# Kernel tuning notes

Measured on AMD Instinct MI355X. Metric: run time of the kernel, lower is better.

## Reference

```python
import jax, jax.numpy as jnp
import numpy as np

N_HEAD = 16
WINDOW = 128
CAUSAL = False


def setup_inputs() -> dict:
    key = jax.random.key(0)
    ks = jax.random.split(key, 5)
    B, T, D = 1, 4096, 1024
    x = jax.random.normal(ks[0], (B, T, D), dtype=jnp.float32)
    w_in = jax.random.normal(ks[1], (3 * D, D), dtype=jnp.float32) * 0.02
    b_in = jax.random.normal(ks[2], (3 * D,), dtype=jnp.float32) * 0.02
    w_out = jax.random.normal(ks[3], (D, D), dtype=jnp.float32) * 0.02
    b_out = jax.random.normal(ks[4], (D,), dtype=jnp.float32) * 0.02
    return {"x": x, "w_in": w_in, "b_in": b_in, "w_out": w_out, "b_out": b_out}


def _window_attention(x, w_in, b_in, w_out, b_out):
    B, T, D = x.shape
    H = N_HEAD
    hd = D // H
    scale = 1.0 / jnp.sqrt(jnp.float32(hd))

    # fused in-projection, as in torch nn.MultiheadAttention (y = x @ W^T + b)
    qkv = jnp.einsum('btd,ed->bte', x, w_in) + b_in  # (B, T, 3D)
    q, k, v = jnp.split(qkv, 3, axis=-1)
    # (B, H, T, hd)
    q = q.reshape(B, T, H, hd).transpose(0, 2, 1, 3)
    k = k.reshape(B, T, H, hd).transpose(0, 2, 1, 3)
    v = v.reshape(B, T, H, hd).transpose(0, 2, 1, 3)

    scores = jnp.einsum('bhqd,bhkd->bhqk', q, k) * scale  # (B, H, T, T)

    idx = jnp.arange(T)
    diff = idx[:, None] - idx[None, :]
    if CAUSAL:
        allowed = (diff >= 0) & (diff <= WINDOW)
    else:
        allowed = jnp.abs(diff) <= WINDOW
    NEG = jnp.float32(-1e30)
    scores = jnp.where(allowed[None, None, :, :], scores, NEG)

    attn = jax.nn.softmax(scores, axis=-1)
    ctx = jnp.einsum('bhqk,bhkd->bhqd', attn, v)  # (B, H, T, hd)
    ctx = ctx.transpose(0, 2, 1, 3).reshape(B, T, D)
    out = jnp.einsum('btd,ed->bte', ctx, w_out) + b_out
    return x + out  # residual, as in the module


def reference(x, w_in, b_in, w_out, b_out):
    return _window_attention(x, w_in, b_in, w_out, b_out)
```

## Files before the change

kernel.cpp:

```cpp
#include <hip/hip_runtime.h>

#define T_SEQ 4096
#define DMODEL 1024
#define NHEAD 16
#define HDIM 64
#define WIN 128

typedef __attribute__((ext_vector_type(8))) short bf16x8;
typedef __attribute__((ext_vector_type(4))) float f32x4;
typedef __attribute__((ext_vector_type(4))) unsigned short u16x4;

__device__ __forceinline__ unsigned short f2bf(float f) {
  unsigned int u = __builtin_bit_cast(unsigned int, f);
  return (unsigned short)((u + 0x7fffu + ((u >> 16) & 1u)) >> 16);
}

__device__ __forceinline__ void gload_lds16(const unsigned short* g,
                                            unsigned short* l) {
  __builtin_amdgcn_global_load_lds(
      (const __attribute__((address_space(1))) void*)g,
      (__attribute__((address_space(3))) void*)l, 16, 0, 0);
}

__global__ void convert_all(const float* __restrict__ x,
                            const float* __restrict__ w_in,
                            const float* __restrict__ w_out,
                            unsigned short* __restrict__ x_bf,
                            unsigned short* __restrict__ w_in_bf,
                            unsigned short* __restrict__ w_out_bf) {
  int stride = gridDim.x * blockDim.x;
  int t0 = blockIdx.x * blockDim.x + threadIdx.x;
#define CVT(SRC, DST, N4)                                          \
  for (int i = t0; i < (N4); i += stride) {                        \
    float4 v = reinterpret_cast<const float4*>(SRC)[i];            \
    u16x4 o;                                                       \
    o.x = f2bf(v.x); o.y = f2bf(v.y); o.z = f2bf(v.z); o.w = f2bf(v.w); \
    reinterpret_cast<u16x4*>(DST)[i] = o;                          \
  }
  CVT(x, x_bf, T_SEQ * DMODEL / 4)
  CVT(w_in, w_in_bf, 3 * DMODEL * DMODEL / 4)
  CVT(w_out, w_out_bf, DMODEL * DMODEL / 4)
#undef CVT
}

template <int EPI, int BM, int BN>
__global__ __launch_bounds__(512) void gemm_db(
    const unsigned short* __restrict__ A,
    const unsigned short* __restrict__ B,
    const float* __restrict__ bias,
    unsigned short* __restrict__ q_buf,
    unsigned short* __restrict__ k_buf,
    unsigned short* __restrict__ vt_buf,
    const float* __restrict__ x_res,
    float* __restrict__ out) {
  const int K = DMODEL;
  constexpr int NT = DMODEL / 64;
  constexpr int SM = 64, SN = BN / 2;
  constexpr int MR = SM / 16, NR = SN / 16;
  constexpr int AL = BM / 64, BL = BN / 64;
  __shared__ __align__(16) unsigned short As[2 * BM * 64];
  __shared__ __align__(16) unsigned short Bs[2 * BN * 64];

  int tid = threadIdx.x;
  int lane = tid & 63, wave = tid >> 6;
  int wr = wave >> 1, wc = wave & 1;
  int lo = lane & 15, hi = lane >> 4;

  int idx = blockIdx.x;
  int xcd = idx & 7, j = idx >> 3;
  int bx = j & 15;
  int by = xcd * 2 + (j >> 4);
  int t0 = by * BM, e0 = bx * BN;

  f32x4 acc[MR][NR];
#pragma unroll
  for (int m = 0; m < MR; ++m)
#pragma unroll
    for (int n = 0; n < NR; ++n) acc[m][n] = (f32x4){0.f, 0.f, 0.f, 0.f};

  int c8 = (tid & 7) ^ ((tid >> 3) & 7);
  int srow = tid >> 3;
  const unsigned short* AbaseG = A + (size_t)(t0 + srow) * K + c8 * 8;
  const unsigned short* BbaseG = B + (size_t)(e0 + srow) * K + c8 * 8;
  unsigned short* ldsAu = As + wave * 512;
  unsigned short* ldsBu = Bs + wave * 512;

  auto stage = [&](int tt) {
    int k0 = tt * 64;
    int ab = (tt & 1) * (BM * 64);
    int bb = (tt & 1) * (BN * 64);
#pragma unroll
    for (int l = 0; l < AL; ++l)
      gload_lds16(AbaseG + (size_t)l * 64 * K + k0, ldsAu + l * 4096 + ab);
#pragma unroll
    for (int l = 0; l < BL; ++l)
      gload_lds16(BbaseG + (size_t)l * 64 * K + k0, ldsBu + l * 4096 + bb);
  };

  stage(0);
  asm volatile("s_waitcnt vmcnt(0) lgkmcnt(0)\n\ts_barrier" ::: "memory");

  for (int t = 0; t < NT; ++t) {
    if (t + 1 < NT) stage(t + 1);
    const unsigned short* Ab = As + (t & 1) * (BM * 64);
    const unsigned short* Bb = Bs + (t & 1) * (BN * 64);
#pragma unroll
    for (int ks = 0; ks < 2; ++ks) {
      bf16x8 af[MR], bfr[NR];
#pragma unroll
      for (int m = 0; m < MR; ++m) {
        int row = wr * SM + m * 16 + lo;
        af[m] = *reinterpret_cast<const bf16x8*>(
            &Ab[row * 64 + (((ks << 2) + hi) ^ (row & 7)) * 8]);
      }
#pragma unroll
      for (int n = 0; n < NR; ++n) {
        int row = wc * SN + n * 16 + lo;
        bfr[n] = *reinterpret_cast<const bf16x8*>(
            &Bb[row * 64 + (((ks << 2) + hi) ^ (row & 7)) * 8]);
      }
#pragma unroll
      for (int m = 0; m < MR; ++m)
#pragma unroll
        for (int n = 0; n < NR; ++n)
          acc[m][n] = __builtin_amdgcn_mfma_f32_16x16x32_bf16(af[m], bfr[n],
                                                              acc[m][n], 0, 0, 0);
    }
    asm volatile("s_waitcnt vmcnt(0) lgkmcnt(0)\n\ts_barrier" ::: "memory");
  }

  int t0w = t0 + wr * SM;
  int e0w = e0 + wc * SN;
#pragma unroll
  for (int m = 0; m < MR; ++m) {
#pragma unroll
    for (int n = 0; n < NR; ++n) {
      int e = e0w + n * 16 + lo;
      float bv = bias[e];
      if (EPI == 0) {
        int part = e >> 10;
        int h = (e >> 6) & 15;
        int d = e & 63;
        if (part == 2) {
          int t = t0w + m * 16 + hi * 4;
          u16x4 pk;
          pk.x = f2bf(acc[m][n][0] + bv);
          pk.y = f2bf(acc[m][n][1] + bv);
          pk.z = f2bf(acc[m][n][2] + bv);
          pk.w = f2bf(acc[m][n][3] + bv);
          *reinterpret_cast<u16x4*>(&vt_buf[((size_t)(h * HDIM + d)) * T_SEQ + t]) = pk;
        } else {
          unsigned short* dst = (part == 0) ? q_buf : k_buf;
#pragma unroll
          for (int jj = 0; jj < 4; ++jj) {
            int t = t0w + m * 16 + hi * 4 + jj;
            dst[((size_t)h * T_SEQ + t) * HDIM + d] = f2bf(acc[m][n][jj] + bv);
          }
        }
      } else {
#pragma unroll
        for (int jj = 0; jj < 4; ++jj) {
          int t = t0w + m * 16 + hi * 4 + jj;
          size_t idxo = (size_t)t * DMODEL + e;
          out[idxo] = acc[m][n][jj] + bv + x_res[idxo];
        }
      }
    }
  }
}

__global__ __launch_bounds__(256) void win_attn(
    const unsigned short* __restrict__ q_buf,
    const unsigned short* __restrict__ k_buf,
    const unsigned short* __restrict__ vt_buf,
    unsigned short* __restrict__ ctx) {
  __shared__ __align__(16) unsigned short p_lds[4][2][16 * 40];
  int tid = threadIdx.x;
  int wave = tid >> 6;
  int lane = tid & 63;
  int lo = lane & 15, hi = lane >> 4;

  int id = blockIdx.x;
  int sw = (id & 7) * (512 / 8) + (id >> 3);
  int job = sw * 4 + wave;
  int h = job >> 7;
  int q0 = (job & 127) * 32;
  const float SC = 0.18033688011112042f;

  bf16x8 aq[2][2];
#pragma unroll
  for (int u = 0; u < 2; ++u) {
    const unsigned short* qrow =
        q_buf + ((size_t)h * T_SEQ + q0 + u * 16 + lo) * HDIM + hi * 8;
    aq[u][0] = *reinterpret_cast<const bf16x8*>(qrow);
    aq[u][1] = *reinterpret_cast<const bf16x8*>(qrow + 32);
  }

  float L[2][4] = {{0.f, 0.f, 0.f, 0.f}, {0.f, 0.f, 0.f, 0.f}};
  f32x4 o[2][4];
#pragma unroll
  for (int u = 0; u < 2; ++u)
#pragma unroll
    for (int n = 0; n < 4; ++n) o[u][n] = (f32x4){0.f, 0.f, 0.f, 0.f};

  int jstart = q0 - WIN; if (jstart < 0) jstart = 0;
  int jend = q0 + 32 + WIN; if (jend > T_SEQ) jend = T_SEQ;

  bf16x8 kc[2][2];
#pragma unroll
  for (int c = 0; c < 2; ++c) {
    const unsigned short* kp =
        k_buf + ((size_t)h * T_SEQ + jstart + c * 16 + lo) * HDIM + hi * 8;
    kc[c][0] = *reinterpret_cast<const bf16x8*>(kp);
    kc[c][1] = *reinterpret_cast<const bf16x8*>(kp + 32);
  }

  for (int j0 = jstart; j0 < jend; j0 += 32) {
    int jn = (j0 + 32 < jend) ? j0 + 32 : jstart;
    bf16x8 kn[2][2];
#pragma unroll
    for (int c = 0; c < 2; ++c) {
      const unsigned short* kp =
          k_buf + ((size_t)h * T_SEQ + jn + c * 16 + lo) * HDIM + hi * 8;
      kn[c][0] = *reinterpret_cast<const bf16x8*>(kp);
      kn[c][1] = *reinterpret_cast<const bf16x8*>(kp + 32);
    }
    bf16x8 bv[4];
#pragma unroll
    for (int n = 0; n < 4; ++n)
      bv[n] = *reinterpret_cast<const bf16x8*>(
          vt_buf + ((size_t)(h * HDIM + n * 16 + lo)) * T_SEQ + j0 + hi * 8);
#pragma unroll
    for (int u = 0; u < 2; ++u) {
#pragma unroll
      for (int c = 0; c < 2; ++c) {
        f32x4 z = (f32x4){0.f, 0.f, 0.f, 0.f};
        z = __builtin_amdgcn_mfma_f32_16x16x32_bf16(aq[u][0], kc[c][0], z, 0, 0, 0);
        z = __builtin_amdgcn_mfma_f32_16x16x32_bf16(aq[u][1], kc[c][1], z, 0, 0, 0);
        int kj = j0 + c * 16 + lo;
#pragma unroll
        for (int jq = 0; jq < 4; ++jq) {
          int q = q0 + u * 16 + hi * 4 + jq;
          bool ok = (q - kj <= WIN) && (kj - q <= WIN);
          float p = ok ? __builtin_amdgcn_exp2f(z[jq] * SC) : 0.f;
          L[u][jq] += p;
          p_lds[wave][u][(hi * 4 + jq) * 40 + c * 16 + lo] = f2bf(p);
        }
      }
    }
    bf16x8 pa[2];
    pa[0] = *reinterpret_cast<const bf16x8*>(&p_lds[wave][0][lo * 40 + hi * 8]);
    pa[1] = *reinterpret_cast<const bf16x8*>(&p_lds[wave][1][lo * 40 + hi * 8]);
#pragma unroll
    for (int n = 0; n < 4; ++n) {
      o[0][n] = __builtin_amdgcn_mfma_f32_16x16x32_bf16(pa[0], bv[n], o[0][n], 0, 0, 0);
      o[1][n] = __builtin_amdgcn_mfma_f32_16x16x32_bf16(pa[1], bv[n], o[1][n], 0, 0, 0);
    }
#pragma unroll
    for (int c = 0; c < 2; ++c) {
      kc[c][0] = kn[c][0];
      kc[c][1] = kn[c][1];
    }
  }
#pragma unroll
  for (int u = 0; u < 2; ++u)
#pragma unroll
    for (int jq = 0; jq < 4; ++jq) {
#pragma unroll
      for (int w = 1; w < 16; w <<= 1) L[u][jq] += __shfl_xor(L[u][jq], w, 64);
    }
#pragma unroll
  for (int u = 0; u < 2; ++u)
#pragma unroll
    for (int jq = 0; jq < 4; ++jq) {
      int t = q0 + u * 16 + hi * 4 + jq;
      float inv = 1.f / L[u][jq];
#pragma unroll
      for (int n = 0; n < 4; ++n)
        ctx[(size_t)t * DMODEL + h * HDIM + n * 16 + lo] = f2bf(o[u][n][jq] * inv);
    }
}

extern "C" void kernel_launch(void* const* d_in, const int* in_sizes, int n_in,
                              void* d_out, int out_size, void* d_ws, size_t ws_size,
                              hipStream_t stream) {
  const float* x = (const float*)d_in[0];
  const float* w_in = (const float*)d_in[1];
  const float* b_in = (const float*)d_in[2];
  const float* w_out = (const float*)d_in[3];
  const float* b_out = (const float*)d_in[4];
  float* out = (float*)d_out;

  char* ws = (char*)d_ws;
  size_t off = 0;
  auto take = [&](size_t bytes) {
    char* p = ws + off;
    off += (bytes + 255) & ~(size_t)255;
    return p;
  };
  unsigned short* x_bf = (unsigned short*)take((size_t)T_SEQ * DMODEL * 2);
  unsigned short* w_in_bf = (unsigned short*)take((size_t)3 * DMODEL * DMODEL * 2);
  unsigned short* w_out_bf = (unsigned short*)take((size_t)DMODEL * DMODEL * 2);
  unsigned short* q_buf = (unsigned short*)take((size_t)T_SEQ * DMODEL * 2);
  unsigned short* k_buf = (unsigned short*)take((size_t)T_SEQ * DMODEL * 2);
  unsigned short* vt_buf = (unsigned short*)take((size_t)T_SEQ * DMODEL * 2 + 8192);
  unsigned short* ctx = (unsigned short*)take((size_t)T_SEQ * DMODEL * 2);

  convert_all<<<2048, 256, 0, stream>>>(x, w_in, w_out, x_bf, w_in_bf, w_out_bf);

  gemm_db<0, 256, 192><<<256, 512, 0, stream>>>(x_bf, w_in_bf, b_in, q_buf, k_buf,
                                                vt_buf, nullptr, nullptr);

  win_attn<<<512, 256, 0, stream>>>(q_buf, k_buf, vt_buf, ctx);

  gemm_db<1, 256, 64><<<256, 512, 0, stream>>>(ctx, w_out_bf, b_out, nullptr, nullptr,
                                               nullptr, x, out);
}
```

Before: 89.48 us.

## Switch GEMMs to triple-buffered K=32 pipeline with partial vmcnt waits

Both projection GEMMs now load 32-wide K slices into a three-deep LDS ring, issuing the load two steps ahead. Each step waits only on the oldest outstanding loads instead of draining all memory ops, so global loads can overlap the MFMA work. MFMA sections are wrapped in s_setprio, and the XCD-aware block swizzle is replaced by a plain 2D grid. The risks are more barriers per K step, per-wave hand-counted vmcnt values that must match the uneven load counts, and possibly worse L2 locality from dropping the swizzle.

```diff
diff --git a/kernel.cpp b/kernel.cpp
--- a/kernel.cpp
+++ b/kernel.cpp
@@ -44,7 +44,7 @@
 }
 
 template <int EPI, int BM, int BN>
-__global__ __launch_bounds__(512) void gemm_db(
+__global__ __launch_bounds__(512) void gemm_p3(
     const unsigned short* __restrict__ A,
     const unsigned short* __restrict__ B,
     const float* __restrict__ bias,
@@ -54,23 +54,21 @@
     const float* __restrict__ x_res,
     float* __restrict__ out) {
   const int K = DMODEL;
-  constexpr int NT = DMODEL / 64;
+  constexpr int NT = DMODEL / 32;
   constexpr int SM = 64, SN = BN / 2;
   constexpr int MR = SM / 16, NR = SN / 16;
-  constexpr int AL = BM / 64, BL = BN / 64;
-  __shared__ __align__(16) unsigned short As[2 * BM * 64];
-  __shared__ __align__(16) unsigned short Bs[2 * BN * 64];
+  constexpr int ALF = BM / 128;
+  constexpr int BLF = BN / 128;
+  constexpr bool BH = (BN % 128) != 0;
+  constexpr int ASZ = BM * 32, BSZ = BN * 32;
+  __shared__ __align__(16) unsigned short As[3 * ASZ];
+  __shared__ __align__(16) unsigned short Bs[3 * BSZ];
 
   int tid = threadIdx.x;
   int lane = tid & 63, wave = tid >> 6;
   int wr = wave >> 1, wc = wave & 1;
   int lo = lane & 15, hi = lane >> 4;
-
-  int idx = blockIdx.x;
-  int xcd = idx & 7, j = idx >> 3;
-  int bx = j & 15;
-  int by = xcd * 2 + (j >> 4);
-  int t0 = by * BM, e0 = bx * BN;
+  int t0 = blockIdx.y * BM, e0 = blockIdx.x * BN;
 
   f32x4 acc[MR][NR];
 #pragma unroll
@@ -78,56 +76,77 @@
 #pragma unroll
     for (int n = 0; n < NR; ++n) acc[m][n] = (f32x4){0.f, 0.f, 0.f, 0.f};
 
-  int c8 = (tid & 7) ^ ((tid >> 3) & 7);
-  int srow = tid >> 3;
-  const unsigned short* AbaseG = A + (size_t)(t0 + srow) * K + c8 * 8;
-  const unsigned short* BbaseG = B + (size_t)(e0 + srow) * K + c8 * 8;
-  unsigned short* ldsAu = As + wave * 512;
-  unsigned short* ldsBu = Bs + wave * 512;
-
-  auto stage = [&](int tt) {
-    int k0 = tt * 64;
-    int ab = (tt & 1) * (BM * 64);
-    int bb = (tt & 1) * (BN * 64);
-#pragma unroll
-    for (int l = 0; l < AL; ++l)
-      gload_lds16(AbaseG + (size_t)l * 64 * K + k0, ldsAu + l * 4096 + ab);
-#pragma unroll
-    for (int l = 0; l < BL; ++l)
-      gload_lds16(BbaseG + (size_t)l * 64 * K + k0, ldsBu + l * 4096 + bb);
+  int srow = tid >> 2;
+  int c8 = (tid & 3) ^ (srow & 3);
+  const unsigned short* AG = A + (size_t)(t0 + srow) * K + c8 * 8;
+  const unsigned short* BG = B + (size_t)(e0 + srow) * K + c8 * 8;
+  const bool bhw = BH && (wave < 4);
+
+  auto stage = [&](int tt, int buf) {
+    int k0 = tt * 32;
+#pragma unroll
+    for (int l = 0; l < ALF; ++l)
+      gload_lds16(AG + (size_t)l * 128 * K + k0,
+                  As + buf * ASZ + l * 4096 + wave * 512);
+#pragma unroll
+    for (int l = 0; l < BLF; ++l)
+      gload_lds16(BG + (size_t)l * 128 * K + k0,
+                  Bs + buf * BSZ + l * 4096 + wave * 512);
+    if (bhw)
+      gload_lds16(BG + (size_t)BLF * 128 * K + k0,
+                  Bs + buf * BSZ + BLF * 4096 + wave * 512);
   };
 
-  stage(0);
-  asm volatile("s_waitcnt vmcnt(0) lgkmcnt(0)\n\ts_barrier" ::: "memory");
-
-  for (int t = 0; t < NT; ++t) {
-    if (t + 1 < NT) stage(t + 1);
-    const unsigned short* Ab = As + (t & 1) * (BM * 64);
-    const unsigned short* Bb = Bs + (t & 1) * (BN * 64);
-#pragma unroll
-    for (int ks = 0; ks < 2; ++ks) {
-      bf16x8 af[MR], bfr[NR];
-#pragma unroll
-      for (int m = 0; m < MR; ++m) {
-        int row = wr * SM + m * 16 + lo;
-        af[m] = *reinterpret_cast<const bf16x8*>(
-            &Ab[row * 64 + (((ks << 2) + hi) ^ (row & 7)) * 8]);
-      }
-#pragma unroll
-      for (int n = 0; n < NR; ++n) {
-        int row = wc * SN + n * 16 + lo;
-        bfr[n] = *reinterpret_cast<const bf16x8*>(
-            &Bb[row * 64 + (((ks << 2) + hi) ^ (row & 7)) * 8]);
-      }
-#pragma unroll
-      for (int m = 0; m < MR; ++m)
-#pragma unroll
-        for (int n = 0; n < NR; ++n)
-          acc[m][n] = __builtin_amdgcn_mfma_f32_16x16x32_bf16(af[m], bfr[n],
-                                                              acc[m][n], 0, 0, 0);
-    }
-    asm volatile("s_waitcnt vmcnt(0) lgkmcnt(0)\n\ts_barrier" ::: "memory");
-  }
+  auto compute = [&](int buf) {
+    const unsigned short* Ab = As + buf * ASZ;
+    const unsigned short* Bb = Bs + buf * BSZ;
+    bf16x8 af[MR], bfr[NR];
+#pragma unroll
+    for (int m = 0; m < MR; ++m) {
+      int row = wr * SM + m * 16 + lo;
+      af[m] = *reinterpret_cast<const bf16x8*>(
+          &Ab[row * 32 + (hi ^ (row & 3)) * 8]);
+    }
+#pragma unroll
+    for (int n = 0; n < NR; ++n) {
+      int row = wc * SN + n * 16 + lo;
+      bfr[n] = *reinterpret_cast<const bf16x8*>(
+          &Bb[row * 32 + (hi ^ (row & 3)) * 8]);
+    }
+    __builtin_amdgcn_s_setprio(1);
+#pragma unroll
+    for (int m = 0; m < MR; ++m)
+#pragma unroll
+      for (int n = 0; n < NR; ++n)
+        acc[m][n] = __builtin_amdgcn_mfma_f32_16x16x32_bf16(af[m], bfr[n],
+                                                            acc[m][n], 0, 0, 0);
+    __builtin_amdgcn_s_setprio(0);
+  };
+
+  stage(0, 0);
+  stage(1, 1);
+  int b0 = 0, b1 = 1, b2 = 2;
+
+#define WBAR(NN) asm volatile("s_waitcnt vmcnt(" #NN ") lgkmcnt(0)\n\ts_barrier" ::: "memory")
+  for (int t = 0; t < NT - 2; ++t) {
+    if constexpr (BN == 192) {
+      if (wave < 4) WBAR(4); else WBAR(3);
+    } else {
+      if (wave < 4) WBAR(3); else WBAR(2);
+    }
+    stage(t + 2, b2);
+    compute(b0);
+    int tmp = b0; b0 = b1; b1 = b2; b2 = tmp;
+  }
+  if constexpr (BN == 192) {
+    if (wave < 4) WBAR(4); else WBAR(3);
+  } else {
+    if (wave < 4) WBAR(3); else WBAR(2);
+  }
+  compute(b0);
+  WBAR(0);
+  compute(b1);
+#undef WBAR
 
   int t0w = t0 + wr * SM;
   int e0w = e0 + wc * SN;
@@ -308,11 +327,13 @@
 
   convert_all<<<2048, 256, 0, stream>>>(x, w_in, w_out, x_bf, w_in_bf, w_out_bf);
 
-  gemm_db<0, 256, 192><<<256, 512, 0, stream>>>(x_bf, w_in_bf, b_in, q_buf, k_buf,
-                                                vt_buf, nullptr, nullptr);
+  dim3 g1(3 * DMODEL / 192, T_SEQ / 256);
+  gemm_p3<0, 256, 192><<<g1, 512, 0, stream>>>(x_bf, w_in_bf, b_in, q_buf, k_buf,
+                                               vt_buf, nullptr, nullptr);
 
   win_attn<<<512, 256, 0, stream>>>(q_buf, k_buf, vt_buf, ctx);
 
-  gemm_db<1, 256, 64><<<256, 512, 0, stream>>>(ctx, w_out_bf, b_out, nullptr, nullptr,
-                                               nullptr, x, out);
-}
+  dim3 g2(DMODEL / 64, T_SEQ / 256);
+  gemm_p3<1, 256, 64><<<g2, 512, 0, stream>>>(ctx, w_out_bf, b_out, nullptr, nullptr,
+                                              nullptr, x, out);
+}
```

Result: slower. 101.1 us (+13.0%).

## Shrink GEMM tiles to 4-wave blocks, prefetch V and add MFMA priority in attention

Applied to the files above, without the earlier changes.

Both projection GEMMs now use 128-row tiles with 256-thread blocks on a plain 2D grid, replacing the 256-row, 512-thread tiles and the XCD-aware block swizzle. This doubles the block count to improve occupancy and load balance, at the cost of less data reuse per tile and losing L2 locality from the swizzle. The GEMM inner loop now loads both k-substeps of fragments before issuing MFMAs. The attention kernel prefetches the next V tile alongside K one iteration ahead and wraps its MFMA groups in s_setprio to favour matrix issue.

```diff
diff --git a/kernel.cpp b/kernel.cpp
--- a/kernel.cpp
+++ b/kernel.cpp
@@ -44,7 +44,7 @@
 }
 
 template <int EPI, int BM, int BN>
-__global__ __launch_bounds__(512) void gemm_db(
+__device__ __forceinline__ void gemm_body(
     const unsigned short* __restrict__ A,
     const unsigned short* __restrict__ B,
     const float* __restrict__ bias,
@@ -55,9 +55,9 @@
     float* __restrict__ out) {
   const int K = DMODEL;
   constexpr int NT = DMODEL / 64;
-  constexpr int SM = 64, SN = BN / 2;
+  constexpr int SM = BM / 2, SN = BN / 2;
   constexpr int MR = SM / 16, NR = SN / 16;
-  constexpr int AL = BM / 64, BL = BN / 64;
+  constexpr int AL = BM / 32, BL = BN / 32;
   __shared__ __align__(16) unsigned short As[2 * BM * 64];
   __shared__ __align__(16) unsigned short Bs[2 * BN * 64];
 
@@ -65,12 +65,7 @@
   int lane = tid & 63, wave = tid >> 6;
   int wr = wave >> 1, wc = wave & 1;
   int lo = lane & 15, hi = lane >> 4;
-
-  int idx = blockIdx.x;
-  int xcd = idx & 7, j = idx >> 3;
-  int bx = j & 15;
-  int by = xcd * 2 + (j >> 4);
-  int t0 = by * BM, e0 = bx * BN;
+  int t0 = blockIdx.y * BM, e0 = blockIdx.x * BN;
 
   f32x4 acc[MR][NR];
 #pragma unroll
@@ -91,10 +86,10 @@
     int bb = (tt & 1) * (BN * 64);
 #pragma unroll
     for (int l = 0; l < AL; ++l)
-      gload_lds16(AbaseG + (size_t)l * 64 * K + k0, ldsAu + l * 4096 + ab);
+      gload_lds16(AbaseG + (size_t)l * 32 * K + k0, ldsAu + l * 2048 + ab);
 #pragma unroll
     for (int l = 0; l < BL; ++l)
-      gload_lds16(BbaseG + (size_t)l * 64 * K + k0, ldsBu + l * 4096 + bb);
+      gload_lds16(BbaseG + (size_t)l * 32 * K + k0, ldsBu + l * 2048 + bb);
   };
 
   stage(0);
@@ -104,28 +99,31 @@
     if (t + 1 < NT) stage(t + 1);
     const unsigned short* Ab = As + (t & 1) * (BM * 64);
     const unsigned short* Bb = Bs + (t & 1) * (BN * 64);
-#pragma unroll
-    for (int ks = 0; ks < 2; ++ks) {
-      bf16x8 af[MR], bfr[NR];
-#pragma unroll
-      for (int m = 0; m < MR; ++m) {
-        int row = wr * SM + m * 16 + lo;
-        af[m] = *reinterpret_cast<const bf16x8*>(
+    bf16x8 af[MR][2], bfr[NR][2];
+#pragma unroll
+    for (int m = 0; m < MR; ++m) {
+      int row = wr * SM + m * 16 + lo;
+#pragma unroll
+      for (int ks = 0; ks < 2; ++ks)
+        af[m][ks] = *reinterpret_cast<const bf16x8*>(
             &Ab[row * 64 + (((ks << 2) + hi) ^ (row & 7)) * 8]);
-      }
-#pragma unroll
-      for (int n = 0; n < NR; ++n) {
-        int row = wc * SN + n * 16 + lo;
-        bfr[n] = *reinterpret_cast<const bf16x8*>(
+    }
+#pragma unroll
+    for (int n = 0; n < NR; ++n) {
+      int row = wc * SN + n * 16 + lo;
+#pragma unroll
+      for (int ks = 0; ks < 2; ++ks)
+        bfr[n][ks] = *reinterpret_cast<const bf16x8*>(
             &Bb[row * 64 + (((ks << 2) + hi) ^ (row & 7)) * 8]);
-      }
+    }
+#pragma unroll
+    for (int ks = 0; ks < 2; ++ks)
 #pragma unroll
       for (int m = 0; m < MR; ++m)
 #pragma unroll
         for (int n = 0; n < NR; ++n)
-          acc[m][n] = __builtin_amdgcn_mfma_f32_16x16x32_bf16(af[m], bfr[n],
+          acc[m][n] = __builtin_amdgcn_mfma_f32_16x16x32_bf16(af[m][ks], bfr[n][ks],
                                                               acc[m][n], 0, 0, 0);
-    }
     asm volatile("s_waitcnt vmcnt(0) lgkmcnt(0)\n\ts_barrier" ::: "memory");
   }
 
@@ -169,6 +167,20 @@
   }
 }
 
+__global__ __launch_bounds__(256) void qkv_gemm(
+    const unsigned short* __restrict__ A, const unsigned short* __restrict__ B,
+    const float* __restrict__ bias, unsigned short* __restrict__ q_buf,
+    unsigned short* __restrict__ k_buf, unsigned short* __restrict__ vt_buf) {
+  gemm_body<0, 128, 192>(A, B, bias, q_buf, k_buf, vt_buf, nullptr, nullptr);
+}
+
+__global__ __launch_bounds__(256) void out_gemm(
+    const unsigned short* __restrict__ A, const unsigned short* __restrict__ B,
+    const float* __restrict__ bias, const float* __restrict__ x_res,
+    float* __restrict__ out) {
+  gemm_body<1, 128, 64>(A, B, bias, nullptr, nullptr, nullptr, x_res, out);
+}
+
 __global__ __launch_bounds__(256) void win_attn(
     const unsigned short* __restrict__ q_buf,
     const unsigned short* __restrict__ k_buf,
@@ -206,7 +218,7 @@
   int jstart = q0 - WIN; if (jstart < 0) jstart = 0;
   int jend = q0 + 32 + WIN; if (jend > T_SEQ) jend = T_SEQ;
 
-  bf16x8 kc[2][2];
+  bf16x8 kc[2][2], vc[4];
 #pragma unroll
   for (int c = 0; c < 2; ++c) {
     const unsigned short* kp =
@@ -214,10 +226,14 @@
     kc[c][0] = *reinterpret_cast<const bf16x8*>(kp);
     kc[c][1] = *reinterpret_cast<const bf16x8*>(kp + 32);
   }
+#pragma unroll
+  for (int n = 0; n < 4; ++n)
+    vc[n] = *reinterpret_cast<const bf16x8*>(
+        vt_buf + ((size_t)(h * HDIM + n * 16 + lo)) * T_SEQ + jstart + hi * 8);
 
   for (int j0 = jstart; j0 < jend; j0 += 32) {
     int jn = (j0 + 32 < jend) ? j0 + 32 : jstart;
-    bf16x8 kn[2][2];
+    bf16x8 kn[2][2], vn[4];
 #pragma unroll
     for (int c = 0; c < 2; ++c) {
       const unsigned short* kp =
@@ -225,18 +241,19 @@
       kn[c][0] = *reinterpret_cast<const bf16x8*>(kp);
       kn[c][1] = *reinterpret_cast<const bf16x8*>(kp + 32);
     }
-    bf16x8 bv[4];
 #pragma unroll
     for (int n = 0; n < 4; ++n)
-      bv[n] = *reinterpret_cast<const bf16x8*>(
-          vt_buf + ((size_t)(h * HDIM + n * 16 + lo)) * T_SEQ + j0 + hi * 8);
+      vn[n] = *reinterpret_cast<const bf16x8*>(
+          vt_buf + ((size_t)(h * HDIM + n * 16 + lo)) * T_SEQ + jn + hi * 8);
 #pragma unroll
     for (int u = 0; u < 2; ++u) {
 #pragma unroll
       for (int c = 0; c < 2; ++c) {
         f32x4 z = (f32x4){0.f, 0.f, 0.f, 0.f};
+        __builtin_amdgcn_s_setprio(1);
         z = __builtin_amdgcn_mfma_f32_16x16x32_bf16(aq[u][0], kc[c][0], z, 0, 0, 0);
         z = __builtin_amdgcn_mfma_f32_16x16x32_bf16(aq[u][1], kc[c][1], z, 0, 0, 0);
+        __builtin_amdgcn_s_setprio(0);
         int kj = j0 + c * 16 + lo;
 #pragma unroll
         for (int jq = 0; jq < 4; ++jq) {
@@ -251,16 +268,20 @@
     bf16x8 pa[2];
     pa[0] = *reinterpret_cast<const bf16x8*>(&p_lds[wave][0][lo * 40 + hi * 8]);
     pa[1] = *reinterpret_cast<const bf16x8*>(&p_lds[wave][1][lo * 40 + hi * 8]);
+    __builtin_amdgcn_s_setprio(1);
 #pragma unroll
     for (int n = 0; n < 4; ++n) {
-      o[0][n] = __builtin_amdgcn_mfma_f32_16x16x32_bf16(pa[0], bv[n], o[0][n], 0, 0, 0);
-      o[1][n] = __builtin_amdgcn_mfma_f32_16x16x32_bf16(pa[1], bv[n], o[1][n], 0, 0, 0);
-    }
+      o[0][n] = __builtin_amdgcn_mfma_f32_16x16x32_bf16(pa[0], vc[n], o[0][n], 0, 0, 0);
+      o[1][n] = __builtin_amdgcn_mfma_f32_16x16x32_bf16(pa[1], vc[n], o[1][n], 0, 0, 0);
+    }
+    __builtin_amdgcn_s_setprio(0);
 #pragma unroll
     for (int c = 0; c < 2; ++c) {
       kc[c][0] = kn[c][0];
       kc[c][1] = kn[c][1];
     }
+#pragma unroll
+    for (int n = 0; n < 4; ++n) vc[n] = vn[n];
   }
 #pragma unroll
   for (int u = 0; u < 2; ++u)
@@ -308,11 +329,11 @@
 
   convert_all<<<2048, 256, 0, stream>>>(x, w_in, w_out, x_bf, w_in_bf, w_out_bf);
 
-  gemm_db<0, 256, 192><<<256, 512, 0, stream>>>(x_bf, w_in_bf, b_in, q_buf, k_buf,
-                                                vt_buf, nullptr, nullptr);
+  dim3 g1(3 * DMODEL / 192, T_SEQ / 128);
+  qkv_gemm<<<g1, 256, 0, stream>>>(x_bf, w_in_bf, b_in, q_buf, k_buf, vt_buf);
 
   win_attn<<<512, 256, 0, stream>>>(q_buf, k_buf, vt_buf, ctx);
 
-  gemm_db<1, 256, 64><<<256, 512, 0, stream>>>(ctx, w_out_bf, b_out, nullptr, nullptr,
-                                               nullptr, x, out);
-}
+  dim3 g2(DMODEL / 64, T_SEQ / 128);
+  out_gemm<<<g2, 256, 0, stream>>>(ctx, w_out_bf, b_out, x, out);
+}
```

New measurement: 89.84 us. Within noise of the previous version (+0.4%).
